# Kernel tuning notes

Measured on AMD Instinct MI355X. Metric: run time of the kernel, lower is better.

The kernel has to match this reference:

```python
import jax, jax.numpy as jnp
import numpy as np

VOCAB = 100000
E = 300          # embedding_size
S = 128          # seq_len
B = 8192         # batch
H1 = 2048
H2 = 2048
C = 1221         # num_classes
PAD = 1          # padding token id (sentence trimmed after last non-1 token)


def setup_inputs() -> dict:
    key = jax.random.key(0)
    ks = jax.random.split(key, 8)
    x = jax.random.randint(ks[0], (S, B), 0, VOCAB, dtype=jnp.int64 if jax.config.jax_enable_x64 else jnp.int32)
    emb = jax.random.normal(ks[1], (VOCAB, E), dtype=jnp.float32) * 0.1
    W1 = jax.random.normal(ks[2], (H1, 2 * E), dtype=jnp.float32) * (1.0 / np.sqrt(2 * E))
    b1 = jnp.zeros((H1,), dtype=jnp.float32)
    W2 = jax.random.normal(ks[3], (H2, H1), dtype=jnp.float32) * (1.0 / np.sqrt(H1))
    b2 = jnp.zeros((H2,), dtype=jnp.float32)
    W_out = jax.random.normal(ks[4], (C, H2), dtype=jnp.float32) * (1.0 / np.sqrt(H2))
    b_out = jnp.zeros((C,), dtype=jnp.float32)
    return {"x": x, "emb": emb, "W1": W1, "b1": b1, "W2": W2, "b2": b2,
            "W_out": W_out, "b_out": b_out}


def reference(x, emb, W1, b1, W2, b2, W_out, b_out):
    # x: [S, B] token ids -> transpose to [B, S] as in torch forward
    xb = x.T                                   # [B, S]
    nonpad = xb != PAD                         # [B, S]
    # index of LAST non-padding token per sentence (torch: (sent != 1).nonzero()[-1])
    last = (S - 1) - jnp.argmax(nonpad[:, ::-1], axis=1)      # [B]
    pos = jnp.arange(S)
    # sentence[:last+1] keeps everything up to and including `last`,
    # including any PAD tokens inside that prefix (faithful to the slice).
    mask = (pos[None, :] <= last[:, None]).astype(emb.dtype)  # [B, S]

    ex = emb[xb]                               # [B, S, E] embedding lookup
    mean = jnp.einsum('bse,bs->be', ex, mask) / jnp.sum(mask, axis=1, keepdims=True)
    feat = jnp.concatenate([ex[:, 0, :], mean], axis=1)       # [B, 2E] (FEE + avg)

    h = jax.nn.relu(feat @ W1.T + b1)          # [B, H1]
    h = jax.nn.relu(h @ W2.T + b2)             # [B, H2]
    out = h @ W_out.T + b_out                  # [B, C]
    return out
```

## Files before the change

### kernel.cpp

```cpp
#include <hip/hip_runtime.h>
#include <hip/hip_bf16.h>

#define S 128
#define BATCH 8192
#define E 300
#define KPAD 640
#define H1 2048
#define H2 2048
#define CLS 1221
#define CPAD 1280
#define PADTOK 1
#define VOCAB 100000

typedef __bf16 bf16x8 __attribute__((ext_vector_type(8)));
typedef float f32x4 __attribute__((ext_vector_type(4)));

__device__ __forceinline__ float b2f(ushort u) {
  union { unsigned int i; float f; } v; v.i = ((unsigned int)u) << 16; return v.f;
}
__device__ __forceinline__ ushort f2b(float f) {
  unsigned int i = __float_as_uint(f);
  unsigned int r = (i + 0x7FFFu + ((i >> 16) & 1u)) >> 16;
  return (ushort)r;
}
__device__ __forceinline__ void async16(const void* g, void* l) {
  __builtin_amdgcn_global_load_lds(
      (__attribute__((address_space(1))) void*)(void*)(const_cast<void*>(g)),
      (__attribute__((address_space(3))) void*)l, 16, 0, 0);
}

__global__ __launch_bounds__(256) void cvt_w1(const float* __restrict__ W1,
                                              ushort* __restrict__ W1p) {
  int idx = blockIdx.x * 256 + threadIdx.x;
  if (idx >= H1 * KPAD) return;
  int h = idx / KPAD;
  int k = idx - h * KPAD;
  W1p[idx] = (k < 2 * E) ? f2b(W1[h * (2 * E) + k]) : (ushort)0;
}

__global__ __launch_bounds__(256) void cvt_w2(const float* __restrict__ W2,
                                              ushort* __restrict__ W2b) {
  int idx = blockIdx.x * 256 + threadIdx.x;
  if (idx >= H2 * H1) return;
  W2b[idx] = f2b(W2[idx]);
}

__global__ __launch_bounds__(256) void cvt_wout(const float* __restrict__ W,
                                                ushort* __restrict__ Wp) {
  int idx = blockIdx.x * 256 + threadIdx.x;
  if (idx >= CPAD * H2) return;
  int n = idx >> 11;
  Wp[idx] = (n < CLS) ? f2b(W[idx]) : (ushort)0;
}

__global__ __launch_bounds__(256) void cvt_emb(const float* __restrict__ Ein,
                                               ushort* __restrict__ Eb) {
  int idx = blockIdx.x * 256 + threadIdx.x;
  const int total = VOCAB * E / 4;
  if (idx >= total) return;
  float4 v = ((const float4*)Ein)[idx];
  ushort4 o;
  o.x = f2b(v.x); o.y = f2b(v.y); o.z = f2b(v.z); o.w = f2b(v.w);
  ((ushort4*)Eb)[idx] = o;
}

__global__ __launch_bounds__(128) void embed_kernel(const int* __restrict__ x,
                                                    const ushort* __restrict__ emb,
                                                    ushort* __restrict__ feat) {
  __shared__ int toks[S];
  __shared__ unsigned long long masks[2];
  const int b = blockIdx.x;
  const int t = threadIdx.x;

  int tok = x[(size_t)t * BATCH + b];
  toks[t] = tok;
  unsigned long long m = __ballot(tok != PADTOK);
  if ((t & 63) == 0) masks[t >> 6] = m;
  __syncthreads();

  unsigned long long m0 = masks[0], m1 = masks[1];
  int last;
  if (m1)      last = 127 - __clzll(m1);
  else if (m0) last = 63 - __clzll(m0);
  else         last = S - 1;
  const int n = last + 1;
  const float inv = 1.0f / (float)n;

  const int p0 = t;
  const int p1 = t + 128;
  const bool has2 = (p1 < E / 2);
  float a0 = 0.f, a1 = 0.f, a2 = 0.f, a3 = 0.f;

  int s = 0;
  for (; s + 8 <= n; s += 8) {
    const ushort* r[8];
#pragma unroll
    for (int j = 0; j < 8; j++) r[j] = emb + (size_t)toks[s + j] * E;
    ushort2 u[8];
#pragma unroll
    for (int j = 0; j < 8; j++) u[j] = *(const ushort2*)(r[j] + 2 * p0);
    ushort2 v[8];
    if (has2) {
#pragma unroll
      for (int j = 0; j < 8; j++) v[j] = *(const ushort2*)(r[j] + 2 * p1);
    }
#pragma unroll
    for (int j = 0; j < 8; j++) { a0 += b2f(u[j].x); a1 += b2f(u[j].y); }
    if (has2) {
#pragma unroll
      for (int j = 0; j < 8; j++) { a2 += b2f(v[j].x); a3 += b2f(v[j].y); }
    }
  }
  for (; s < n; s++) {
    const ushort* row = emb + (size_t)toks[s] * E;
    ushort2 u = *(const ushort2*)(row + 2 * p0);
    a0 += b2f(u.x); a1 += b2f(u.y);
    if (has2) {
      ushort2 v0 = *(const ushort2*)(row + 2 * p1);
      a2 += b2f(v0.x); a3 += b2f(v0.y);
    }
  }

  ushort* fr = feat + (size_t)b * KPAD;
  ushort2 mo;
  mo.x = f2b(a0 * inv); mo.y = f2b(a1 * inv);
  *(ushort2*)(fr + E + 2 * p0) = mo;
  if (has2) {
    ushort2 mo2;
    mo2.x = f2b(a2 * inv); mo2.y = f2b(a3 * inv);
    *(ushort2*)(fr + E + 2 * p1) = mo2;
  }
  const ushort* r0 = emb + (size_t)toks[0] * E;
  *(ushort2*)(fr + 2 * p0) = *(const ushort2*)(r0 + 2 * p0);
  if (has2) *(ushort2*)(fr + 2 * p1) = *(const ushort2*)(r0 + 2 * p1);
  if (t < (KPAD - 2 * E) / 2) {
    ushort2 z; z.x = 0; z.y = 0;
    *(ushort2*)(fr + 2 * E + 2 * t) = z;
  }
}

#define BM 128
#define BN 128
#define BK 32

template <bool RELU, bool NGUARD, bool FP32OUT>
__global__ __launch_bounds__(256) void gemm_bt(const ushort* __restrict__ A,
                                               const ushort* __restrict__ B,
                                               const float* __restrict__ bias,
                                               void* __restrict__ Cv,
                                               int K, int lda, int ldb, int ldc,
                                               int Nreal) {
  __shared__ __align__(16) ushort lA[BM * BK];
  __shared__ __align__(16) ushort lB[BN * BK];

  const int tid = threadIdx.x;
  const int wave = tid >> 6;
  const int lane = tid & 63;
  const int m0 = blockIdx.y * BM;
  const int n0 = blockIdx.x * BN;
  const int wm = (wave >> 1) * 64;
  const int wn = (wave & 1) * 64;

  f32x4 acc[4][4];
#pragma unroll
  for (int i = 0; i < 4; i++)
#pragma unroll
    for (int j = 0; j < 4; j++) acc[i][j] = (f32x4){0.f, 0.f, 0.f, 0.f};

  const int srow = lane >> 2;
  const int skel = (lane & 3) * 8;

  const int lrow = lane & 15;
  const int lkel = (lane >> 4) * 8;

  for (int k0 = 0; k0 < K; k0 += BK) {
#pragma unroll
    for (int j = 0; j < 2; j++) {
      const int i = wave * 2 + j;
      const int row = i * 16 + srow;
      async16(A + (size_t)(m0 + row) * lda + k0 + skel, (void*)&lA[i * 512]);
      async16(B + (size_t)(n0 + row) * ldb + k0 + skel, (void*)&lB[i * 512]);
    }
    __syncthreads();

    bf16x8 af[4], bfr[4];
#pragma unroll
    for (int mi = 0; mi < 4; mi++)
      af[mi] = *(const bf16x8*)&lA[(wm + mi * 16 + lrow) * BK + lkel];
#pragma unroll
    for (int ni = 0; ni < 4; ni++)
      bfr[ni] = *(const bf16x8*)&lB[(wn + ni * 16 + lrow) * BK + lkel];
#pragma unroll
    for (int mi = 0; mi < 4; mi++)
#pragma unroll
      for (int ni = 0; ni < 4; ni++)
        acc[mi][ni] = __builtin_amdgcn_mfma_f32_16x16x32_bf16(af[mi], bfr[ni],
                                                              acc[mi][ni], 0, 0, 0);
    __syncthreads();
  }

  const int row_in = (lane >> 4) * 4;
  const int col_in = lane & 15;
#pragma unroll
  for (int ni = 0; ni < 4; ni++) {
    const int col = n0 + wn + ni * 16 + col_in;
    const bool ok = (!NGUARD) || (col < Nreal);
    const float bv = ok ? bias[col] : 0.f;
#pragma unroll
    for (int mi = 0; mi < 4; mi++) {
#pragma unroll
      for (int r = 0; r < 4; r++) {
        const int row = m0 + wm + mi * 16 + row_in + r;
        float v = acc[mi][ni][r] + bv;
        if (RELU) v = fmaxf(v, 0.f);
        if (ok) {
          if (FP32OUT) ((float*)Cv)[(size_t)row * ldc + col] = v;
          else         ((ushort*)Cv)[(size_t)row * ldc + col] = f2b(v);
        }
      }
    }
  }
}

extern "C" void kernel_launch(void* const* d_in, const int* in_sizes, int n_in,
                              void* d_out, int out_size, void* d_ws, size_t ws_size,
                              hipStream_t stream) {
  const int* x = (const int*)d_in[0];
  const float* emb = (const float*)d_in[1];
  const float* W1 = (const float*)d_in[2];
  const float* b1 = (const float*)d_in[3];
  const float* W2 = (const float*)d_in[4];
  const float* b2 = (const float*)d_in[5];
  const float* Wout = (const float*)d_in[6];
  const float* bout = (const float*)d_in[7];
  float* out = (float*)d_out;

  char* ws = (char*)d_ws;
  ushort* feat = (ushort*)ws;  ws += (size_t)BATCH * KPAD * 2;
  ushort* h1 = (ushort*)ws;    ws += (size_t)BATCH * H1 * 2;
  ushort* h2 = (ushort*)ws;    ws += (size_t)BATCH * H2 * 2;
  ushort* W1p = (ushort*)ws;   ws += (size_t)H1 * KPAD * 2;
  ushort* W2b = (ushort*)ws;   ws += (size_t)H2 * H1 * 2;
  ushort* Woutp = (ushort*)ws; ws += (size_t)CPAD * H2 * 2;
  ushort* Eb = (ushort*)ws;    ws += (size_t)VOCAB * E * 2;

  cvt_emb<<<(VOCAB * E / 4 + 255) / 256, 256, 0, stream>>>(emb, Eb);
  cvt_w1<<<(H1 * KPAD + 255) / 256, 256, 0, stream>>>(W1, W1p);
  cvt_w2<<<(H2 * H1 + 255) / 256, 256, 0, stream>>>(W2, W2b);
  cvt_wout<<<(CPAD * H2 + 255) / 256, 256, 0, stream>>>(Wout, Woutp);
  embed_kernel<<<BATCH, S, 0, stream>>>(x, Eb, feat);

  gemm_bt<true, false, false><<<dim3(H1 / BN, BATCH / BM), 256, 0, stream>>>(
      feat, W1p, b1, (void*)h1, KPAD, KPAD, KPAD, H1, H1);
  gemm_bt<true, false, false><<<dim3(H2 / BN, BATCH / BM), 256, 0, stream>>>(
      h1, W2b, b2, (void*)h2, H1, H1, H1, H2, H2);
  gemm_bt<false, true, true><<<dim3(CPAD / BN, BATCH / BM), 256, 0, stream>>>(
      h2, Woutp, bout, (void*)out, H2, H2, H2, CLS, CLS);
}
```

Baseline: 574.2 us.

## Fuse conversion kernels, pre-transpose tokens, and retune embedding gather

Merges the four weight/embedding conversion kernels into a single launch that also writes a batch-major transposed copy of the token ids, and vectorizes the W1/Wout conversions to 4 elements per thread. The embedding kernel reads the transposed tokens contiguously, keeps precomputed byte offsets in shared memory, unrolls the gather loop to 16 rows, and reassigns column pairs so each wavefront's second load is handled by lanes 0-10 of each wave. This cuts launch overhead and strided token reads, at the cost of an extra workspace buffer and a transpose pass with its own strided reads.

```diff
diff --git a/kernel.cpp b/kernel.cpp
--- a/kernel.cpp
+++ b/kernel.cpp
@@ -29,51 +29,85 @@
       (__attribute__((address_space(3))) void*)l, 16, 0, 0);
 }
 
-__global__ __launch_bounds__(256) void cvt_w1(const float* __restrict__ W1,
-                                              ushort* __restrict__ W1p) {
-  int idx = blockIdx.x * 256 + threadIdx.x;
-  if (idx >= H1 * KPAD) return;
-  int h = idx / KPAD;
-  int k = idx - h * KPAD;
-  W1p[idx] = (k < 2 * E) ? f2b(W1[h * (2 * E) + k]) : (ushort)0;
-}
-
-__global__ __launch_bounds__(256) void cvt_w2(const float* __restrict__ W2,
-                                              ushort* __restrict__ W2b) {
-  int idx = blockIdx.x * 256 + threadIdx.x;
-  if (idx >= H2 * H1) return;
-  W2b[idx] = f2b(W2[idx]);
-}
-
-__global__ __launch_bounds__(256) void cvt_wout(const float* __restrict__ W,
-                                                ushort* __restrict__ Wp) {
-  int idx = blockIdx.x * 256 + threadIdx.x;
-  if (idx >= CPAD * H2) return;
-  int n = idx >> 11;
-  Wp[idx] = (n < CLS) ? f2b(W[idx]) : (ushort)0;
-}
-
-__global__ __launch_bounds__(256) void cvt_emb(const float* __restrict__ Ein,
-                                               ushort* __restrict__ Eb) {
-  int idx = blockIdx.x * 256 + threadIdx.x;
-  const int total = VOCAB * E / 4;
-  if (idx >= total) return;
-  float4 v = ((const float4*)Ein)[idx];
-  ushort4 o;
-  o.x = f2b(v.x); o.y = f2b(v.y); o.z = f2b(v.z); o.w = f2b(v.w);
-  ((ushort4*)Eb)[idx] = o;
-}
-
-__global__ __launch_bounds__(128) void embed_kernel(const int* __restrict__ x,
+#define NQ_EMB (VOCAB * E / 4)
+#define NQ_W1  (H1 * KPAD / 4)
+#define NQ_W2  (H1 * H2 / 4)
+#define NQ_WO  (CPAD * H2 / 4)
+#define NQ_XT  (S * BATCH / 4)
+#define NQ_TOT (NQ_EMB + NQ_W1 + NQ_W2 + NQ_WO + NQ_XT)
+
+__global__ __launch_bounds__(256) void cvt_all(const float* __restrict__ Ein,
+                                               ushort* __restrict__ Eb,
+                                               const float* __restrict__ W1,
+                                               ushort* __restrict__ W1p,
+                                               const float* __restrict__ W2,
+                                               ushort* __restrict__ W2b,
+                                               const float* __restrict__ Wout,
+                                               ushort* __restrict__ Woutp,
+                                               const int* __restrict__ x,
+                                               int* __restrict__ xT) {
+  int q = blockIdx.x * 256 + threadIdx.x;
+  if (q < NQ_EMB) {
+    float4 v = ((const float4*)Ein)[q];
+    ushort4 o;
+    o.x = f2b(v.x); o.y = f2b(v.y); o.z = f2b(v.z); o.w = f2b(v.w);
+    ((ushort4*)Eb)[q] = o;
+    return;
+  }
+  q -= NQ_EMB;
+  if (q < NQ_W1) {
+    int row = q / 160;
+    int k0 = (q - row * 160) * 4;
+    ushort4 o; o.x = 0; o.y = 0; o.z = 0; o.w = 0;
+    if (k0 < 2 * E) {
+      float4 v = *(const float4*)(W1 + (size_t)row * (2 * E) + k0);
+      o.x = f2b(v.x); o.y = f2b(v.y); o.z = f2b(v.z); o.w = f2b(v.w);
+    }
+    ((ushort4*)W1p)[q] = o;
+    return;
+  }
+  q -= NQ_W1;
+  if (q < NQ_W2) {
+    float4 v = ((const float4*)W2)[q];
+    ushort4 o;
+    o.x = f2b(v.x); o.y = f2b(v.y); o.z = f2b(v.z); o.w = f2b(v.w);
+    ((ushort4*)W2b)[q] = o;
+    return;
+  }
+  q -= NQ_W2;
+  if (q < NQ_WO) {
+    int n = (q * 4) >> 11;
+    ushort4 o; o.x = 0; o.y = 0; o.z = 0; o.w = 0;
+    if (n < CLS) {
+      float4 v = ((const float4*)Wout)[q];
+      o.x = f2b(v.x); o.y = f2b(v.y); o.z = f2b(v.z); o.w = f2b(v.w);
+    }
+    ((ushort4*)Woutp)[q] = o;
+    return;
+  }
+  q -= NQ_WO;
+  if (q < NQ_XT) {
+    int b = q >> 5;
+    int t4 = (q & 31) * 4;
+    int4 o;
+    o.x = x[(size_t)(t4 + 0) * BATCH + b];
+    o.y = x[(size_t)(t4 + 1) * BATCH + b];
+    o.z = x[(size_t)(t4 + 2) * BATCH + b];
+    o.w = x[(size_t)(t4 + 3) * BATCH + b];
+    ((int4*)xT)[q] = o;
+  }
+}
+
+__global__ __launch_bounds__(128) void embed_kernel(const int* __restrict__ xT,
                                                     const ushort* __restrict__ emb,
                                                     ushort* __restrict__ feat) {
-  __shared__ int toks[S];
+  __shared__ uint offs[S];
   __shared__ unsigned long long masks[2];
   const int b = blockIdx.x;
   const int t = threadIdx.x;
 
-  int tok = x[(size_t)t * BATCH + b];
-  toks[t] = tok;
+  int tok = xT[b * S + t];
+  offs[t] = (uint)tok * 600u;
   unsigned long long m = __ballot(tok != PADTOK);
   if ((t & 63) == 0) masks[t >> 6] = m;
   __syncthreads();
@@ -86,54 +120,56 @@
   const int n = last + 1;
   const float inv = 1.0f / (float)n;
 
-  const int p0 = t;
-  const int p1 = t + 128;
-  const bool has2 = (p1 < E / 2);
+  const int lane = t & 63;
+  const int q0 = (t < 64) ? t : (11 + t);
+  const bool has2 = (lane < 11);
+  const int q1 = q0 + 64;
+  const uint off0 = 4u * (uint)q0;
+  const uint off1 = 4u * (uint)q1;
+  const char* base = (const char*)emb;
+
   float a0 = 0.f, a1 = 0.f, a2 = 0.f, a3 = 0.f;
-
   int s = 0;
-  for (; s + 8 <= n; s += 8) {
-    const ushort* r[8];
-#pragma unroll
-    for (int j = 0; j < 8; j++) r[j] = emb + (size_t)toks[s + j] * E;
-    ushort2 u[8];
-#pragma unroll
-    for (int j = 0; j < 8; j++) u[j] = *(const ushort2*)(r[j] + 2 * p0);
-    ushort2 v[8];
+  for (; s + 16 <= n; s += 16) {
+    uint o[16];
+#pragma unroll
+    for (int j = 0; j < 16; j++) o[j] = offs[s + j];
+    ushort2 u[16];
+#pragma unroll
+    for (int j = 0; j < 16; j++) u[j] = *(const ushort2*)(base + (o[j] + off0));
+    ushort2 v[16];
     if (has2) {
 #pragma unroll
-      for (int j = 0; j < 8; j++) v[j] = *(const ushort2*)(r[j] + 2 * p1);
-    }
-#pragma unroll
-    for (int j = 0; j < 8; j++) { a0 += b2f(u[j].x); a1 += b2f(u[j].y); }
+      for (int j = 0; j < 16; j++) v[j] = *(const ushort2*)(base + (o[j] + off1));
+    }
+#pragma unroll
+    for (int j = 0; j < 16; j++) { a0 += b2f(u[j].x); a1 += b2f(u[j].y); }
     if (has2) {
 #pragma unroll
-      for (int j = 0; j < 8; j++) { a2 += b2f(v[j].x); a3 += b2f(v[j].y); }
+      for (int j = 0; j < 16; j++) { a2 += b2f(v[j].x); a3 += b2f(v[j].y); }
     }
   }
   for (; s < n; s++) {
-    const ushort* row = emb + (size_t)toks[s] * E;
-    ushort2 u = *(const ushort2*)(row + 2 * p0);
+    uint o = offs[s];
+    ushort2 u = *(const ushort2*)(base + (o + off0));
     a0 += b2f(u.x); a1 += b2f(u.y);
     if (has2) {
-      ushort2 v0 = *(const ushort2*)(row + 2 * p1);
+      ushort2 v0 = *(const ushort2*)(base + (o + off1));
       a2 += b2f(v0.x); a3 += b2f(v0.y);
     }
   }
 
   ushort* fr = feat + (size_t)b * KPAD;
-  ushort2 mo;
-  mo.x = f2b(a0 * inv); mo.y = f2b(a1 * inv);
-  *(ushort2*)(fr + E + 2 * p0) = mo;
+  ushort2 mo; mo.x = f2b(a0 * inv); mo.y = f2b(a1 * inv);
+  *(ushort2*)(fr + E + 2 * q0) = mo;
   if (has2) {
-    ushort2 mo2;
-    mo2.x = f2b(a2 * inv); mo2.y = f2b(a3 * inv);
-    *(ushort2*)(fr + E + 2 * p1) = mo2;
-  }
-  const ushort* r0 = emb + (size_t)toks[0] * E;
-  *(ushort2*)(fr + 2 * p0) = *(const ushort2*)(r0 + 2 * p0);
-  if (has2) *(ushort2*)(fr + 2 * p1) = *(const ushort2*)(r0 + 2 * p1);
-  if (t < (KPAD - 2 * E) / 2) {
+    ushort2 mo2; mo2.x = f2b(a2 * inv); mo2.y = f2b(a3 * inv);
+    *(ushort2*)(fr + E + 2 * q1) = mo2;
+  }
+  const uint o0 = offs[0];
+  *(ushort2*)(fr + 2 * q0) = *(const ushort2*)(base + (o0 + off0));
+  if (has2) *(ushort2*)(fr + 2 * q1) = *(const ushort2*)(base + (o0 + off1));
+  if (t < 20) {
     ushort2 z; z.x = 0; z.y = 0;
     *(ushort2*)(fr + 2 * E + 2 * t) = z;
   }
@@ -243,12 +279,11 @@
   ushort* W2b = (ushort*)ws;   ws += (size_t)H2 * H1 * 2;
   ushort* Woutp = (ushort*)ws; ws += (size_t)CPAD * H2 * 2;
   ushort* Eb = (ushort*)ws;    ws += (size_t)VOCAB * E * 2;
-
-  cvt_emb<<<(VOCAB * E / 4 + 255) / 256, 256, 0, stream>>>(emb, Eb);
-  cvt_w1<<<(H1 * KPAD + 255) / 256, 256, 0, stream>>>(W1, W1p);
-  cvt_w2<<<(H2 * H1 + 255) / 256, 256, 0, stream>>>(W2, W2b);
-  cvt_wout<<<(CPAD * H2 + 255) / 256, 256, 0, stream>>>(Wout, Woutp);
-  embed_kernel<<<BATCH, S, 0, stream>>>(x, Eb, feat);
+  int* xT = (int*)ws;          ws += (size_t)S * BATCH * 4;
+
+  cvt_all<<<(NQ_TOT + 255) / 256, 256, 0, stream>>>(emb, Eb, W1, W1p, W2, W2b,
+                                                    Wout, Woutp, x, xT);
+  embed_kernel<<<BATCH, S, 0, stream>>>(xT, Eb, feat);
 
   gemm_bt<true, false, false><<<dim3(H1 / BN, BATCH / BM), 256, 0, stream>>>(
       feat, W1p, b1, (void*)h1, KPAD, KPAD, KPAD, H1, H1);
```

Result: faster. 543.7 us (-5.3%).
